# Kernel tuning notes

Measured on AMD Instinct MI355X. Metric: run time of the kernel, lower is better.

Reference implementation:

```python
import jax, jax.numpy as jnp
import numpy as np

N = 100000      # nodes
E = 1200000     # edges (avg degree ~12)
F_IN = 64       # input feature dim
HID = 64        # hidden_channels
OUT = 64        # out_channels


def setup_inputs() -> dict:
    key = jax.random.key(0)
    ks = jax.random.split(key, 9)
    s_in = 1.0 / np.sqrt(F_IN)
    s_h = 1.0 / np.sqrt(HID)
    inp = {
        "x": jax.random.normal(ks[0], (N, F_IN), dtype=jnp.float32),
        "edge_index": jax.random.randint(ks[1], (2, E), 0, N, dtype=jnp.int64),
        # conv_in: lin_l (with bias) applied to aggregated msgs, lin_r (no bias) to self
        "Wl_in": jax.random.normal(ks[2], (HID, F_IN), dtype=jnp.float32) * s_in,
        "bl_in": jnp.zeros((HID,), dtype=jnp.float32),
        "Wr_in": jax.random.normal(ks[3], (HID, F_IN), dtype=jnp.float32) * s_in,
        # conv_med (shared across the 2 middle applications)
        "Wl_med": jax.random.normal(ks[4], (HID, HID), dtype=jnp.float32) * s_h,
        "bl_med": jnp.zeros((HID,), dtype=jnp.float32),
        "Wr_med": jax.random.normal(ks[5], (HID, HID), dtype=jnp.float32) * s_h,
        # conv_out
        "Wl_out": jax.random.normal(ks[6], (OUT, HID), dtype=jnp.float32) * s_h,
        "bl_out": jnp.zeros((OUT,), dtype=jnp.float32),
        "Wr_out": jax.random.normal(ks[7], (OUT, HID), dtype=jnp.float32) * s_h,
    }
    return inp


def reference(x, edge_index, Wl_in, bl_in, Wr_in, Wl_med, bl_med, Wr_med,
              Wl_out, bl_out, Wr_out):
    src = edge_index[0]
    dst = edge_index[1]
    n = x.shape[0]

    def sage(h, Wl, bl, Wr):
        # sum-aggregate neighbor messages h_j into each destination node i
        agg = jax.ops.segment_sum(h[src], dst, num_segments=n)  # [N, F]
        return agg @ Wl.T + bl + h @ Wr.T

    # eval mode: dropout is identity
    h = jnp.tanh(sage(x, Wl_in, bl_in, Wr_in))
    for _ in range(2):  # conv_med applied twice with shared weights
        h = jnp.tanh(sage(h, Wl_med, bl_med, Wr_med))
    return sage(h, Wl_out, bl_out, Wr_out)
```

## Files before the change

kernel.cpp:

```cpp
#include <hip/hip_runtime.h>
#include <cstdint>

#define F 64
#define TILE1 8192
#define MAXFB 1024
#define SCAN_BLK 1024

typedef short bf16x8 __attribute__((ext_vector_type(8)));
typedef float f32x4  __attribute__((ext_vector_type(4)));

__device__ __forceinline__ unsigned short f2b(float f) {
    unsigned u = __float_as_uint(f);
    unsigned r = u + 0x7fffu + ((u >> 16) & 1u);
    return (unsigned short)(r >> 16);
}
__device__ __forceinline__ void add8(float* a, uint4 u) {
    const unsigned* p = (const unsigned*)&u;
#pragma unroll
    for (int i = 0; i < 4; ++i) {
        a[2 * i + 0] += __uint_as_float(p[i] << 16);
        a[2 * i + 1] += __uint_as_float(p[i] & 0xffff0000u);
    }
}

__global__ __launch_bounds__(256) void hist_kernel(
    const int* __restrict__ dst, int* __restrict__ binMat,
    int E, int NB1, int nf) {
    __shared__ int h[MAXFB];
    int t = threadIdx.x;
    for (int i = t; i < nf; i += 256) h[i] = 0;
    __syncthreads();
    int base = blockIdx.x * TILE1;
    int end = min(base + TILE1, E);
    const int4* d4 = (const int4*)dst;
    int n4 = (end - base) >> 2;
    int b4 = base >> 2;
    for (int k = t; k < n4; k += 256) {
        int4 v = d4[b4 + k];
        atomicAdd(&h[v.x >> 7], 1);
        atomicAdd(&h[v.y >> 7], 1);
        atomicAdd(&h[v.z >> 7], 1);
        atomicAdd(&h[v.w >> 7], 1);
    }
    __syncthreads();
    for (int i = t; i < nf; i += 256) binMat[i * NB1 + blockIdx.x] = h[i];
}

__global__ __launch_bounds__(SCAN_BLK) void scan_blocks_kernel(
    int* __restrict__ a, int* __restrict__ blockSums, int len) {
    __shared__ int sh[SCAN_BLK];
    int t = threadIdx.x;
    int i = blockIdx.x * SCAN_BLK + t;
    int v = (i < len) ? a[i] : 0;
    sh[t] = v;
    __syncthreads();
    for (int off = 1; off < SCAN_BLK; off <<= 1) {
        int add = (t >= off) ? sh[t - off] : 0;
        __syncthreads();
        sh[t] += add;
        __syncthreads();
    }
    int incl = sh[t];
    if (i < len) a[i] = incl - v;
    if (t == SCAN_BLK - 1) blockSums[blockIdx.x] = incl;
}

__global__ __launch_bounds__(SCAN_BLK) void scan_sums_kernel(
    int* __restrict__ blockSums, int nb) {
    __shared__ int sh[SCAN_BLK];
    int t = threadIdx.x;
    int v = (t < nb) ? blockSums[t] : 0;
    sh[t] = v;
    __syncthreads();
    for (int off = 1; off < SCAN_BLK; off <<= 1) {
        int add = (t >= off) ? sh[t - off] : 0;
        __syncthreads();
        sh[t] += add;
        __syncthreads();
    }
    if (t < nb) blockSums[t] = sh[t] - v;
}

__global__ __launch_bounds__(256) void scan_add_kernel(
    int* __restrict__ a, const int* __restrict__ blockSums, int len) {
    int i = blockIdx.x * 256 + threadIdx.x;
    if (i < len) a[i] += blockSums[i >> 10];
}

__global__ __launch_bounds__(256) void scatter_kernel(
    const int* __restrict__ src, const int* __restrict__ dst,
    const int* __restrict__ binMat, unsigned* __restrict__ stage2,
    int E, int NB1, int nf) {
    __shared__ int cur[MAXFB];
    int t = threadIdx.x;
    for (int i = t; i < nf; i += 256) cur[i] = binMat[i * NB1 + blockIdx.x];
    __syncthreads();
    int base = blockIdx.x * TILE1;
    int end = min(base + TILE1, E);
    const int4* s4 = (const int4*)src;
    const int4* d4 = (const int4*)dst;
    int n4 = (end - base) >> 2;
    int b4 = base >> 2;
    for (int k = t; k < n4; k += 256) {
        int4 s = s4[b4 + k];
        int4 d = d4[b4 + k];
        int p0 = atomicAdd(&cur[d.x >> 7], 1);
        int p1 = atomicAdd(&cur[d.y >> 7], 1);
        int p2 = atomicAdd(&cur[d.z >> 7], 1);
        int p3 = atomicAdd(&cur[d.w >> 7], 1);
        stage2[p0] = ((unsigned)(d.x & 127) << 17) | (unsigned)s.x;
        stage2[p1] = ((unsigned)(d.y & 127) << 17) | (unsigned)s.y;
        stage2[p2] = ((unsigned)(d.z & 127) << 17) | (unsigned)s.z;
        stage2[p3] = ((unsigned)(d.w & 127) << 17) | (unsigned)s.w;
    }
}

__global__ __launch_bounds__(256) void phase2_kernel(
    const unsigned* __restrict__ stage2, const int* __restrict__ binMat,
    int* __restrict__ csrSrc, int* __restrict__ rowStart,
    int E, int NB1, int nf) {
    __shared__ int cnt[128];
    __shared__ int pre[129];
    __shared__ int cur[128];
    int b = blockIdx.x;
    int t = threadIdx.x;
    int s = binMat[b * NB1];
    int e2 = (b + 1 < nf) ? binMat[(b + 1) * NB1] : E;
    if (t < 128) cnt[t] = 0;
    __syncthreads();
    for (int i = s + t; i < e2; i += 256)
        atomicAdd(&cnt[(stage2[i] >> 17) & 127], 1);
    __syncthreads();
    if (t < 128) pre[t + 1] = cnt[t];
    if (t == 0) pre[0] = 0;
    __syncthreads();
    for (int off = 1; off < 128; off <<= 1) {
        int v = 0;
        if (t < 128 && (t + 1) > off) v = pre[t + 1 - off];
        __syncthreads();
        if (t < 128 && (t + 1) > off) pre[t + 1] += v;
        __syncthreads();
    }
    if (t < 128) cur[t] = pre[t];
    if (t < 129) rowStart[b * 128 + t] = s + pre[t];
    __syncthreads();
    for (int i = s + t; i < e2; i += 256) {
        unsigned w = stage2[i];
        int pos = atomicAdd(&cur[(w >> 17) & 127], 1);
        csrSrc[s + pos] = (int)(w & 0x1FFFFu);
    }
}

__global__ __launch_bounds__(256) void prep_kernel(
    const float* __restrict__ Wl0, const float* __restrict__ Wr0,
    const float* __restrict__ Wl1, const float* __restrict__ Wr1,
    const float* __restrict__ Wl2, const float* __restrict__ Wr2,
    ushort* __restrict__ wbuf,
    const float* __restrict__ x, ushort* __restrict__ xb, int nElem) {
    int b = blockIdx.x;
    int t = threadIdx.x;
    if (b < 12) {
        int g = b * 256 + t;
        int set = g >> 10;
        int fl = g & 1023;
        int f = fl >> 6;
        int l = fl & 63;
        int s = f >> 2;
        int ot = f & 3;
        const float* Wl = (set == 0) ? Wl0 : (set == 1) ? Wl1 : Wl2;
        const float* Wr = (set == 0) ? Wr0 : (set == 1) ? Wr1 : Wr2;
        int o = ot * 16 + (l & 15);
        int k0 = s * 32 + (l >> 4) * 8;
        unsigned d[4];
#pragma unroll
        for (int p = 0; p < 4; ++p) {
            int ka = k0 + 2 * p, kb = k0 + 2 * p + 1;
            float va = (ka < 64) ? Wl[o * 64 + ka] : Wr[o * 64 + (ka - 64)];
            float vb = (kb < 64) ? Wl[o * 64 + kb] : Wr[o * 64 + (kb - 64)];
            d[p] = (unsigned)f2b(va) | ((unsigned)f2b(vb) << 16);
        }
        ((uint4*)wbuf)[g] = make_uint4(d[0], d[1], d[2], d[3]);
    } else {
        int i = (b - 12) * 256 + t;
        int n4 = nElem >> 2;
        if (i < n4) {
            float4 v = ((const float4*)x)[i];
            uint2 o;
            o.x = (unsigned)f2b(v.x) | ((unsigned)f2b(v.y) << 16);
            o.y = (unsigned)f2b(v.z) | ((unsigned)f2b(v.w) << 16);
            ((uint2*)xb)[i] = o;
        }
    }
}

__global__ __launch_bounds__(256, 4) void fused_layer(
    const ushort* __restrict__ hb, const int* __restrict__ rowStart,
    const int* __restrict__ csrSrc, const ushort* __restrict__ wbuf,
    const float* __restrict__ bl, void* __restrict__ out, int n, int flags) {
    __shared__ __align__(16) ushort smem[128 * 72];

    int t = threadIdx.x;
    int node0b = blockIdx.x * 128;
    const uint4* h16 = (const uint4*)hb;

    {
        int c = t & 7;
        int nlb = t >> 3;
#pragma unroll 1
        for (int r = 0; r < 4; ++r) {
            int nl = r * 32 + nlb;
            int node = node0b + nl;
            float a[8] = {0.f, 0.f, 0.f, 0.f, 0.f, 0.f, 0.f, 0.f};
            int e = rowStart[node];
            int end = rowStart[node + 1];
            for (; e + 3 < end; e += 4) {
                int s0 = csrSrc[e + 0];
                int s1 = csrSrc[e + 1];
                int s2 = csrSrc[e + 2];
                int s3 = csrSrc[e + 3];
                uint4 u0 = h16[(size_t)s0 * 8 + c];
                uint4 u1 = h16[(size_t)s1 * 8 + c];
                uint4 u2 = h16[(size_t)s2 * 8 + c];
                uint4 u3 = h16[(size_t)s3 * 8 + c];
                add8(a, u0); add8(a, u1); add8(a, u2); add8(a, u3);
            }
            for (; e < end; ++e) {
                uint4 u0 = h16[(size_t)csrSrc[e] * 8 + c];
                add8(a, u0);
            }
            unsigned d[4];
#pragma unroll
            for (int p = 0; p < 4; ++p)
                d[p] = (unsigned)f2b(a[2 * p]) | ((unsigned)f2b(a[2 * p + 1]) << 16);
            *(uint4*)(smem + nl * 72 + c * 8) = make_uint4(d[0], d[1], d[2], d[3]);
        }
    }
    __syncthreads();

    int w = t >> 6;
    int l = t & 63;
    int quad = l >> 4;
    int lo = l & 15;

    f32x4 acc[2][4];
#pragma unroll
    for (int ot = 0; ot < 4; ++ot) {
        float bv = bl[ot * 16 + lo];
        f32x4 bvv = {bv, bv, bv, bv};
        acc[0][ot] = bvv;
        acc[1][ot] = bvv;
    }

#pragma unroll
    for (int s = 0; s < 4; ++s) {
        bf16x8 A[2];
#pragma unroll
        for (int mt = 0; mt < 2; ++mt) {
            if (s < 2) {
                int nl = w * 32 + mt * 16 + lo;
                A[mt] = *(const bf16x8*)(smem + nl * 72 + s * 32 + quad * 8);
            } else {
                size_t node = (size_t)node0b + w * 32 + mt * 16 + lo;
                A[mt] = *(const bf16x8*)(hb + node * 64 + (s & 1) * 32 + quad * 8);
            }
        }
#pragma unroll
        for (int ot = 0; ot < 4; ++ot) {
            bf16x8 B = *(const bf16x8*)(wbuf + (((s * 4 + ot) * 64) + l) * 8);
#pragma unroll
            for (int mt = 0; mt < 2; ++mt)
                acc[mt][ot] = __builtin_amdgcn_mfma_f32_16x16x32_bf16(
                    A[mt], B, acc[mt][ot], 0, 0, 0);
        }
    }
    __syncthreads();

    float* outT = (float*)smem;
    int whalf = w >> 1;
    int wrow = (w & 1) * 32;

#pragma unroll
    for (int half = 0; half < 2; ++half) {
        if (whalf == half) {
#pragma unroll
            for (int mt = 0; mt < 2; ++mt) {
#pragma unroll
                for (int ot = 0; ot < 4; ++ot) {
                    f32x4 v = acc[mt][ot];
                    if (flags & 1) {
                        v[0] = tanhf(v[0]); v[1] = tanhf(v[1]);
                        v[2] = tanhf(v[2]); v[3] = tanhf(v[3]);
                    }
                    int row = wrow + mt * 16 + quad * 4;
                    int col = ot * 16 + lo;
#pragma unroll
                    for (int r = 0; r < 4; ++r)
                        outT[(row + r) * 68 + col] = v[r];
                }
            }
        }
        __syncthreads();
        int hr = t >> 2;
        int node = node0b + half * 64 + hr;
        if (node < n) {
            const float* srcp = &outT[hr * 68 + (t & 3) * 16];
            if (flags & 2) {
                uint4* o8 = (uint4*)out;
#pragma unroll
                for (int q = 0; q < 2; ++q) {
                    unsigned dd[4];
#pragma unroll
                    for (int p = 0; p < 4; ++p) {
                        float va = srcp[q * 8 + 2 * p];
                        float vb = srcp[q * 8 + 2 * p + 1];
                        dd[p] = (unsigned)f2b(va) | ((unsigned)f2b(vb) << 16);
                    }
                    o8[(size_t)node * 8 + (t & 3) * 2 + q] =
                        make_uint4(dd[0], dd[1], dd[2], dd[3]);
                }
            } else {
                float4* o16 = (float4*)out;
#pragma unroll
                for (int q = 0; q < 4; ++q) {
                    float4 v = *(const float4*)(srcp + q * 4);
                    o16[(size_t)node * 16 + (t & 3) * 4 + q] = v;
                }
            }
        }
        if (half == 0) __syncthreads();
    }
}

extern "C" void kernel_launch(void* const* d_in, const int* in_sizes, int n_in,
                              void* d_out, int out_size, void* d_ws, size_t ws_size,
                              hipStream_t stream) {
    const float* x      = (const float*)d_in[0];
    const int*   edges  = (const int*)d_in[1];
    const float* Wl_in  = (const float*)d_in[2];
    const float* bl_in  = (const float*)d_in[3];
    const float* Wr_in  = (const float*)d_in[4];
    const float* Wl_med = (const float*)d_in[5];
    const float* bl_med = (const float*)d_in[6];
    const float* Wr_med = (const float*)d_in[7];
    const float* Wl_out = (const float*)d_in[8];
    const float* bl_out = (const float*)d_in[9];
    const float* Wr_out = (const float*)d_in[10];

    const int N = in_sizes[0] / F;
    const int E = in_sizes[1] / 2;
    const int* src = edges;
    const int* dst = edges + E;

    const int nf  = (N + 127) >> 7;
    const int NB1 = (E + TILE1 - 1) / TILE1;
    const int NR  = nf * 128;
    const int scanLen = nf * NB1;
    const int nbScan = (scanLen + SCAN_BLK - 1) / SCAN_BLK;

    ushort*  wbuf      = (ushort*)d_ws;
    ushort*  xb        = wbuf + 3 * 8192;
    ushort*  hAb       = xb + (size_t)NR * F;
    ushort*  hBb       = hAb + (size_t)NR * F;
    int*     rowStart  = (int*)(hBb + (size_t)NR * F);
    int*     blockSums = rowStart + NR + 2;
    int*     binMat    = blockSums + SCAN_BLK;
    unsigned* stage2   = (unsigned*)(binMat + scanLen);
    int*     csrSrc    = (int*)(stage2 + E);

    const int prep_blocks = 12 + (N * F / 4 + 255) / 256;

    prep_kernel<<<prep_blocks, 256, 0, stream>>>(Wl_in, Wr_in, Wl_med, Wr_med,
                                                 Wl_out, Wr_out, wbuf, x, xb, N * F);

    hist_kernel<<<NB1, 256, 0, stream>>>(dst, binMat, E, NB1, nf);
    scan_blocks_kernel<<<nbScan, SCAN_BLK, 0, stream>>>(binMat, blockSums, scanLen);
    scan_sums_kernel<<<1, SCAN_BLK, 0, stream>>>(blockSums, nbScan);
    scan_add_kernel<<<(scanLen + 255) / 256, 256, 0, stream>>>(binMat, blockSums, scanLen);
    scatter_kernel<<<NB1, 256, 0, stream>>>(src, dst, binMat, stage2, E, NB1, nf);
    phase2_kernel<<<nf, 256, 0, stream>>>(stage2, binMat, csrSrc, rowStart, E, NB1, nf);

    fused_layer<<<nf, 256, 0, stream>>>(xb,  rowStart, csrSrc, wbuf,         bl_in,  hAb,   N, 3);
    fused_layer<<<nf, 256, 0, stream>>>(hAb, rowStart, csrSrc, wbuf + 8192,  bl_med, hBb,   N, 3);
    fused_layer<<<nf, 256, 0, stream>>>(hBb, rowStart, csrSrc, wbuf + 8192,  bl_med, hAb,   N, 3);
    fused_layer<<<nf, 256, 0, stream>>>(hAb, rowStart, csrSrc, wbuf + 16384, bl_out, d_out, N, 0);
}
```

Measured before the change: 297.0 us.

## Merge prep with histogram, fold scan-add into consumers, use 512-thread layer blocks

The weight/feature prep kernel and the destination histogram kernel become one launch. The separate scan_add pass is removed: scatter and phase2 now add the block-sum offset themselves when they read binMat. The fused layer kernel moves from 256 to 512 threads per block, with each wave handling one 16-row MFMA tile instead of two, which aims to get more parallelism into the gather and the store. The changes cut two launches and add warps, but each wave now has less work to amortise weight loads.

Result: faster. 269.7 us (-9.2%).

```diff
diff --git a/kernel.cpp b/kernel.cpp
--- a/kernel.cpp
+++ b/kernel.cpp
@@ -23,27 +23,67 @@
     }
 }
 
-__global__ __launch_bounds__(256) void hist_kernel(
+__global__ __launch_bounds__(256) void prep_hist_kernel(
+    const float* __restrict__ Wl0, const float* __restrict__ Wr0,
+    const float* __restrict__ Wl1, const float* __restrict__ Wr1,
+    const float* __restrict__ Wl2, const float* __restrict__ Wr2,
+    ushort* __restrict__ wbuf,
+    const float* __restrict__ x, ushort* __restrict__ xb, int nElem,
     const int* __restrict__ dst, int* __restrict__ binMat,
     int E, int NB1, int nf) {
     __shared__ int h[MAXFB];
-    int t = threadIdx.x;
-    for (int i = t; i < nf; i += 256) h[i] = 0;
-    __syncthreads();
-    int base = blockIdx.x * TILE1;
-    int end = min(base + TILE1, E);
-    const int4* d4 = (const int4*)dst;
-    int n4 = (end - base) >> 2;
-    int b4 = base >> 2;
-    for (int k = t; k < n4; k += 256) {
-        int4 v = d4[b4 + k];
-        atomicAdd(&h[v.x >> 7], 1);
-        atomicAdd(&h[v.y >> 7], 1);
-        atomicAdd(&h[v.z >> 7], 1);
-        atomicAdd(&h[v.w >> 7], 1);
-    }
-    __syncthreads();
-    for (int i = t; i < nf; i += 256) binMat[i * NB1 + blockIdx.x] = h[i];
+    int b = blockIdx.x;
+    int t = threadIdx.x;
+    if (b < 12) {
+        int g = b * 256 + t;
+        int set = g >> 10;
+        int fl = g & 1023;
+        int f = fl >> 6;
+        int l = fl & 63;
+        int s = f >> 2;
+        int ot = f & 3;
+        const float* Wl = (set == 0) ? Wl0 : (set == 1) ? Wl1 : Wl2;
+        const float* Wr = (set == 0) ? Wr0 : (set == 1) ? Wr1 : Wr2;
+        int o = ot * 16 + (l & 15);
+        int k0 = s * 32 + (l >> 4) * 8;
+        unsigned d[4];
+#pragma unroll
+        for (int p = 0; p < 4; ++p) {
+            int ka = k0 + 2 * p, kb = k0 + 2 * p + 1;
+            float va = (ka < 64) ? Wl[o * 64 + ka] : Wr[o * 64 + (ka - 64)];
+            float vb = (kb < 64) ? Wl[o * 64 + kb] : Wr[o * 64 + (kb - 64)];
+            d[p] = (unsigned)f2b(va) | ((unsigned)f2b(vb) << 16);
+        }
+        ((uint4*)wbuf)[g] = make_uint4(d[0], d[1], d[2], d[3]);
+    } else if (b < 12 + NB1) {
+        int tb = b - 12;
+        for (int i = t; i < nf; i += 256) h[i] = 0;
+        __syncthreads();
+        int base = tb * TILE1;
+        int end = min(base + TILE1, E);
+        const int4* d4 = (const int4*)dst;
+        int n4 = (end - base) >> 2;
+        int b4 = base >> 2;
+        for (int k = t; k < n4; k += 256) {
+            int4 v = d4[b4 + k];
+            atomicAdd(&h[v.x >> 7], 1);
+            atomicAdd(&h[v.y >> 7], 1);
+            atomicAdd(&h[v.z >> 7], 1);
+            atomicAdd(&h[v.w >> 7], 1);
+        }
+        __syncthreads();
+        for (int i = t; i < nf; i += 256) binMat[i * NB1 + tb] = h[i];
+    } else {
+        int i = (b - 12 - NB1) * 256 + t;
+        int n4 = nElem >> 2;
+        if (i < n4) {
+            float4 v = ((const float4*)x)[i];
+            uint2 o;
+            o.x = (unsigned)f2b(v.x) | ((unsigned)f2b(v.y) << 16);
+            o.y = (unsigned)f2b(v.z) | ((unsigned)f2b(v.w) << 16);
+            ((uint2*)xb)[i] = o;
+        }
+    }
 }
 
 __global__ __launch_bounds__(SCAN_BLK) void scan_blocks_kernel(
@@ -81,19 +121,16 @@
     if (t < nb) blockSums[t] = sh[t] - v;
 }
 
-__global__ __launch_bounds__(256) void scan_add_kernel(
-    int* __restrict__ a, const int* __restrict__ blockSums, int len) {
-    int i = blockIdx.x * 256 + threadIdx.x;
-    if (i < len) a[i] += blockSums[i >> 10];
-}
-
 __global__ __launch_bounds__(256) void scatter_kernel(
     const int* __restrict__ src, const int* __restrict__ dst,
-    const int* __restrict__ binMat, unsigned* __restrict__ stage2,
-    int E, int NB1, int nf) {
+    const int* __restrict__ binMat, const int* __restrict__ blockSums,
+    unsigned* __restrict__ stage2, int E, int NB1, int nf) {
     __shared__ int cur[MAXFB];
     int t = threadIdx.x;
-    for (int i = t; i < nf; i += 256) cur[i] = binMat[i * NB1 + blockIdx.x];
+    for (int i = t; i < nf; i += 256) {
+        int j = i * NB1 + blockIdx.x;
+        cur[i] = binMat[j] + blockSums[j >> 10];
+    }
     __syncthreads();
     int base = blockIdx.x * TILE1;
     int end = min(base + TILE1, E);
@@ -117,6 +154,7 @@
 
 __global__ __launch_bounds__(256) void phase2_kernel(
     const unsigned* __restrict__ stage2, const int* __restrict__ binMat,
+    const int* __restrict__ blockSums,
     int* __restrict__ csrSrc, int* __restrict__ rowStart,
     int E, int NB1, int nf) {
     __shared__ int cnt[128];
@@ -124,8 +162,13 @@
     __shared__ int cur[128];
     int b = blockIdx.x;
     int t = threadIdx.x;
-    int s = binMat[b * NB1];
-    int e2 = (b + 1 < nf) ? binMat[(b + 1) * NB1] : E;
+    int j0 = b * NB1;
+    int s = binMat[j0] + blockSums[j0 >> 10];
+    int e2 = E;
+    if (b + 1 < nf) {
+        int j1 = (b + 1) * NB1;
+        e2 = binMat[j1] + blockSums[j1 >> 10];
+    }
     if (t < 128) cnt[t] = 0;
     __syncthreads();
     for (int i = s + t; i < e2; i += 256)
@@ -151,49 +194,7 @@
     }
 }
 
-__global__ __launch_bounds__(256) void prep_kernel(
-    const float* __restrict__ Wl0, const float* __restrict__ Wr0,
-    const float* __restrict__ Wl1, const float* __restrict__ Wr1,
-    const float* __restrict__ Wl2, const float* __restrict__ Wr2,
-    ushort* __restrict__ wbuf,
-    const float* __restrict__ x, ushort* __restrict__ xb, int nElem) {
-    int b = blockIdx.x;
-    int t = threadIdx.x;
-    if (b < 12) {
-        int g = b * 256 + t;
-        int set = g >> 10;
-        int fl = g & 1023;
-        int f = fl >> 6;
-        int l = fl & 63;
-        int s = f >> 2;
-        int ot = f & 3;
-        const float* Wl = (set == 0) ? Wl0 : (set == 1) ? Wl1 : Wl2;
-        const float* Wr = (set == 0) ? Wr0 : (set == 1) ? Wr1 : Wr2;
-        int o = ot * 16 + (l & 15);
-        int k0 = s * 32 + (l >> 4) * 8;
-        unsigned d[4];
-#pragma unroll
-        for (int p = 0; p < 4; ++p) {
-            int ka = k0 + 2 * p, kb = k0 + 2 * p + 1;
-            float va = (ka < 64) ? Wl[o * 64 + ka] : Wr[o * 64 + (ka - 64)];
-            float vb = (kb < 64) ? Wl[o * 64 + kb] : Wr[o * 64 + (kb - 64)];
-            d[p] = (unsigned)f2b(va) | ((unsigned)f2b(vb) << 16);
-        }
-        ((uint4*)wbuf)[g] = make_uint4(d[0], d[1], d[2], d[3]);
-    } else {
-        int i = (b - 12) * 256 + t;
-        int n4 = nElem >> 2;
-        if (i < n4) {
-            float4 v = ((const float4*)x)[i];
-            uint2 o;
-            o.x = (unsigned)f2b(v.x) | ((unsigned)f2b(v.y) << 16);
-            o.y = (unsigned)f2b(v.z) | ((unsigned)f2b(v.w) << 16);
-            ((uint2*)xb)[i] = o;
-        }
-    }
-}
-
-__global__ __launch_bounds__(256, 4) void fused_layer(
+__global__ __launch_bounds__(512, 4) void fused_layer(
     const ushort* __restrict__ hb, const int* __restrict__ rowStart,
     const int* __restrict__ csrSrc, const ushort* __restrict__ wbuf,
     const float* __restrict__ bl, void* __restrict__ out, int n, int flags) {
@@ -207,8 +208,8 @@
         int c = t & 7;
         int nlb = t >> 3;
 #pragma unroll 1
-        for (int r = 0; r < 4; ++r) {
-            int nl = r * 32 + nlb;
+        for (int r = 0; r < 2; ++r) {
+            int nl = r * 64 + nlb;
             int node = node0b + nl;
             float a[8] = {0.f, 0.f, 0.f, 0.f, 0.f, 0.f, 0.f, 0.f};
             int e = rowStart[node];
@@ -242,88 +243,74 @@
     int quad = l >> 4;
     int lo = l & 15;
 
-    f32x4 acc[2][4];
+    f32x4 acc[4];
 #pragma unroll
     for (int ot = 0; ot < 4; ++ot) {
         float bv = bl[ot * 16 + lo];
         f32x4 bvv = {bv, bv, bv, bv};
-        acc[0][ot] = bvv;
-        acc[1][ot] = bvv;
+        acc[ot] = bvv;
     }
 
 #pragma unroll
     for (int s = 0; s < 4; ++s) {
-        bf16x8 A[2];
-#pragma unroll
-        for (int mt = 0; mt < 2; ++mt) {
-            if (s < 2) {
-                int nl = w * 32 + mt * 16 + lo;
-                A[mt] = *(const bf16x8*)(smem + nl * 72 + s * 32 + quad * 8);
-            } else {
-                size_t node = (size_t)node0b + w * 32 + mt * 16 + lo;
-                A[mt] = *(const bf16x8*)(hb + node * 64 + (s & 1) * 32 + quad * 8);
-            }
+        bf16x8 A;
+        if (s < 2) {
+            int nl = w * 16 + lo;
+            A = *(const bf16x8*)(smem + nl * 72 + s * 32 + quad * 8);
+        } else {
+            size_t node = (size_t)node0b + w * 16 + lo;
+            A = *(const bf16x8*)(hb + node * 64 + (s & 1) * 32 + quad * 8);
         }
 #pragma unroll
         for (int ot = 0; ot < 4; ++ot) {
             bf16x8 B = *(const bf16x8*)(wbuf + (((s * 4 + ot) * 64) + l) * 8);
-#pragma unroll
-            for (int mt = 0; mt < 2; ++mt)
-                acc[mt][ot] = __builtin_amdgcn_mfma_f32_16x16x32_bf16(
-                    A[mt], B, acc[mt][ot], 0, 0, 0);
+            acc[ot] = __builtin_amdgcn_mfma_f32_16x16x32_bf16(A, B, acc[ot], 0, 0, 0);
         }
     }
     __syncthreads();
 
     float* outT = (float*)smem;
-    int whalf = w >> 1;
-    int wrow = (w & 1) * 32;
+    int whalf = w >> 2;
+    int wrow = (w & 3) * 16;
 
 #pragma unroll
     for (int half = 0; half < 2; ++half) {
         if (whalf == half) {
 #pragma unroll
-            for (int mt = 0; mt < 2; ++mt) {
-#pragma unroll
-                for (int ot = 0; ot < 4; ++ot) {
-                    f32x4 v = acc[mt][ot];
-                    if (flags & 1) {
-                        v[0] = tanhf(v[0]); v[1] = tanhf(v[1]);
-                        v[2] = tanhf(v[2]); v[3] = tanhf(v[3]);
-                    }
-                    int row = wrow + mt * 16 + quad * 4;
-                    int col = ot * 16 + lo;
-#pragma unroll
-                    for (int r = 0; r < 4; ++r)
-                        outT[(row + r) * 68 + col] = v[r];
+            for (int ot = 0; ot < 4; ++ot) {
+                f32x4 v = acc[ot];
+                if (flags & 1) {
+                    v[0] = tanhf(v[0]); v[1] = tanhf(v[1]);
+                    v[2] = tanhf(v[2]); v[3] = tanhf(v[3]);
                 }
+                int row = wrow + quad * 4;
+                int col = ot * 16 + lo;
+#pragma unroll
+                for (int r = 0; r < 4; ++r)
+                    outT[(row + r) * 68 + col] = v[r];
             }
         }
         __syncthreads();
-        int hr = t >> 2;
+        int hr = t >> 3;
         int node = node0b + half * 64 + hr;
         if (node < n) {
-            const float* srcp = &outT[hr * 68 + (t & 3) * 16];
+            const float* srcp = &outT[hr * 68 + (t & 7) * 8];
             if (flags & 2) {
                 uint4* o8 = (uint4*)out;
-#pragma unroll
-                for (int q = 0; q < 2; ++q) {
-                    unsigned dd[4];
-#pragma unroll
-                    for (int p = 0; p < 4; ++p) {
-                        float va = srcp[q * 8 + 2 * p];
-                        float vb = srcp[q * 8 + 2 * p + 1];
-                        dd[p] = (unsigned)f2b(va) | ((unsigned)f2b(vb) << 16);
-                    }
-                    o8[(size_t)node * 8 + (t & 3) * 2 + q] =
-                        make_uint4(dd[0], dd[1], dd[2], dd[3]);
+                unsigned dd[4];
+#pragma unroll
+                for (int p = 0; p < 4; ++p) {
+                    float va = srcp[2 * p];
+                    float vb = srcp[2 * p + 1];
+                    dd[p] = (unsigned)f2b(va) | ((unsigned)f2b(vb) << 16);
                 }
+                o8[(size_t)node * 8 + (t & 7)] = make_uint4(dd[0], dd[1], dd[2], dd[3]);
             } else {
                 float4* o16 = (float4*)out;
 #pragma unroll
-                for (int q = 0; q < 4; ++q) {
+                for (int q = 0; q < 2; ++q) {
                     float4 v = *(const float4*)(srcp + q * 4);
-                    o16[(size_t)node * 16 + (t & 3) * 4 + q] = v;
+                    o16[(size_t)node * 16 + (t & 7) * 2 + q] = v;
                 }
             }
         }
@@ -367,20 +354,18 @@
     unsigned* stage2   = (unsigned*)(binMat + scanLen);
     int*     csrSrc    = (int*)(stage2 + E);
 
-    const int prep_blocks = 12 + (N * F / 4 + 255) / 256;
-
-    prep_kernel<<<prep_blocks, 256, 0, stream>>>(Wl_in, Wr_in, Wl_med, Wr_med,
-                                                 Wl_out, Wr_out, wbuf, x, xb, N * F);
-
-    hist_kernel<<<NB1, 256, 0, stream>>>(dst, binMat, E, NB1, nf);
+    const int prep_blocks = 12 + NB1 + (N * F / 4 + 255) / 256;
+
+    prep_hist_kernel<<<prep_blocks, 256, 0, stream>>>(
+        Wl_in, Wr_in, Wl_med, Wr_med, Wl_out, Wr_out, wbuf, x, xb, N * F,
+        dst, binMat, E, NB1, nf);
     scan_blocks_kernel<<<nbScan, SCAN_BLK, 0, stream>>>(binMat, blockSums, scanLen);
     scan_sums_kernel<<<1, SCAN_BLK, 0, stream>>>(blockSums, nbScan);
-    scan_add_kernel<<<(scanLen + 255) / 256, 256, 0, stream>>>(binMat, blockSums, scanLen);
-    scatter_kernel<<<NB1, 256, 0, stream>>>(src, dst, binMat, stage2, E, NB1, nf);
-    phase2_kernel<<<nf, 256, 0, stream>>>(stage2, binMat, csrSrc, rowStart, E, NB1, nf);
-
-    fused_layer<<<nf, 256, 0, stream>>>(xb,  rowStart, csrSrc, wbuf,         bl_in,  hAb,   N, 3);
-    fused_layer<<<nf, 256, 0, stream>>>(hAb, rowStart, csrSrc, wbuf + 8192,  bl_med, hBb,   N, 3);
-    fused_layer<<<nf, 256, 0, stream>>>(hBb, rowStart, csrSrc, wbuf + 8192,  bl_med, hAb,   N, 3);
-    fused_layer<<<nf, 256, 0, stream>>>(hAb, rowStart, csrSrc, wbuf + 16384, bl_out, d_out, N, 0);
-}
+    scatter_kernel<<<NB1, 256, 0, stream>>>(src, dst, binMat, blockSums, stage2, E, NB1, nf);
+    phase2_kernel<<<nf, 256, 0, stream>>>(stage2, binMat, blockSums, csrSrc, rowStart, E, NB1, nf);
+
+    fused_layer<<<nf, 512, 0, stream>>>(xb,  rowStart, csrSrc, wbuf,         bl_in,  hAb,   N, 3);
+    fused_layer<<<nf, 512, 0, stream>>>(hAb, rowStart, csrSrc, wbuf + 8192,  bl_med, hBb,   N, 3);
+    fused_layer<<<nf, 512, 0, stream>>>(hBb, rowStart, csrSrc, wbuf + 8192,  bl_med, hAb,   N, 3);
+    fused_layer<<<nf, 512, 0, stream>>>(hAb, rowStart, csrSrc, wbuf + 16384, bl_out, d_out, N, 0);
+}
```
